# Performance work log

Measured on AMD Instinct MI355X. Metric: run time of the kernel, lower is better.

## Reference

```python
import jax, jax.numpy as jnp
import numpy as np

N_CTX = 4096
D_MODEL = 2048
D_HEAD = 128


def setup_inputs() -> dict:
    key = jax.random.key(0)
    k1, k2, k3, k4 = jax.random.split(key, 4)
    x = jax.random.normal(k1, (N_CTX, D_MODEL), dtype=jnp.float32)
    # torch nn.Linear weights are [out, in]; kept in that layout.
    Wk = jax.random.normal(k2, (D_HEAD, D_MODEL), dtype=jnp.float32) * (1.0 / np.sqrt(D_MODEL))
    Wq = jax.random.normal(k3, (D_HEAD, D_MODEL), dtype=jnp.float32) * (1.0 / np.sqrt(D_MODEL))
    W2 = jax.random.normal(k4, (D_MODEL, D_MODEL), dtype=jnp.float32) * (1.0 / np.sqrt(D_MODEL))
    return {"x": x, "Wk": Wk, "Wq": Wq, "W2": W2}


def reference(x, Wk, Wq, W2):
    # Faithful to the torch module: no 1/sqrt(d_head) scaling, V = x itself.
    n = x.shape[0]
    q = x @ Wq.T                     # [n, d_head]
    k = x @ Wk.T                     # [n, d_head]
    scores = q @ k.T                 # [n, n]
    # causal mask: strictly-upper-triangular entries -> -inf
    causal = jnp.tril(jnp.ones((n, n), dtype=bool))
    scores = jnp.where(causal, scores, -jnp.inf)
    attn = jax.nn.softmax(scores, axis=1)  # [n, n]
    out = attn @ x                   # [n, d_model] (V is the raw input)
    return out @ W2.T                # [n, d_model]
```

## Files before the change

kernel.cpp:

```cpp
#include <hip/hip_runtime.h>

#define NCTX 4096
#define DMODEL 2048
#define DHEAD 128

typedef _Float16 f16;
typedef f16 f16x8 __attribute__((ext_vector_type(8)));
typedef float f32x4 __attribute__((ext_vector_type(4)));
typedef unsigned short u16;
typedef u16 u16x8 __attribute__((ext_vector_type(8)));

__device__ __forceinline__ u16 f2h(float f) {
  union { f16 h; u16 u; } v; v.h = (f16)f; return v.u;
}
__device__ __forceinline__ float h2f(u16 u) {
  union { u16 u; f16 h; } v; v.u = u; return (float)v.h;
}

__device__ __forceinline__ void gl_lds16(const void* g, void* l) {
  __builtin_amdgcn_global_load_lds((const __attribute__((address_space(1))) void*)g,
                                   (__attribute__((address_space(3))) void*)l, 16, 0, 0);
}

__device__ __forceinline__ void splitH4(float4 v, ushort4& h, ushort4& l) {
  h.x = f2h(v.x); l.x = f2h(v.x - h2f(h.x));
  h.y = f2h(v.y); l.y = f2h(v.y - h2f(h.y));
  h.z = f2h(v.z); l.z = f2h(v.z - h2f(h.z));
  h.w = f2h(v.w); l.w = f2h(v.w - h2f(h.w));
}

__global__ __launch_bounds__(256) void prep_all(const float* __restrict__ x,
                                                const float* __restrict__ Wq,
                                                const float* __restrict__ Wk,
                                                const float* __restrict__ W2,
                                                u16* __restrict__ xh, u16* __restrict__ xl,
                                                u16* __restrict__ Wf, u16* __restrict__ W2f,
                                                u16* __restrict__ XT) {
  __shared__ float tile[64][65];
  int b = blockIdx.x;
  int t = threadIdx.x;
  if (b < 2048) {
    int mb = (b >> 5) * 64, db = (b & 31) * 64;
    int tx = t & 15, ty = t >> 4;
#pragma unroll
    for (int rr = 0; rr < 4; ++rr) {
      int row = rr * 16 + ty;
      float4 v = *(const float4*)(x + (size_t)(mb + row) * DMODEL + db + tx * 4);
      ushort4 h, l; splitH4(v, h, l);
      size_t gi = ((size_t)(mb + row) * DMODEL + db) / 4 + tx;
      ((ushort4*)xh)[gi] = h; ((ushort4*)xl)[gi] = l;
      tile[row][tx * 4 + 0] = v.x; tile[row][tx * 4 + 1] = v.y;
      tile[row][tx * 4 + 2] = v.z; tile[row][tx * 4 + 3] = v.w;
    }
    __syncthreads();
#pragma unroll
    for (int rr = 0; rr < 4; ++rr) {
      int r = (t >> 4) * 4 + rr;
      int c0 = (t & 15) * 4;
      ushort4 o;
      o.x = f2h(tile[c0 + 0][r]); o.y = f2h(tile[c0 + 1][r]);
      o.z = f2h(tile[c0 + 2][r]); o.w = f2h(tile[c0 + 3][r]);
      *(ushort4*)(XT + (size_t)(db + r) * NCTX + mb + c0) = o;
    }
  } else if (b < 2560) {
    int wk = (b >= 2304);
    int i = (b - (wk ? 2304 : 2048)) * 256 + t;
    const float* W = wk ? Wk : Wq;
    size_t off = wk ? ((size_t)DHEAD * DMODEL / 4) : 0;
    float4 v = ((const float4*)W)[i];
    ushort4 o;
    o.x = f2h(v.x); o.y = f2h(v.y); o.z = f2h(v.z); o.w = f2h(v.w);
    ((ushort4*)Wf)[off + i] = o;
  } else {
    int i = (b - 2560) * 256 + t;
    float4 v = ((const float4*)W2)[i];
    ushort4 o;
    o.x = f2h(v.x); o.y = f2h(v.y); o.z = f2h(v.z); o.w = f2h(v.w);
    ((ushort4*)W2f)[i] = o;
  }
}

__global__ __launch_bounds__(256) void reduce8h(const u16* __restrict__ P,
                                                u16* __restrict__ out, int n8) {
  int i = blockIdx.x * 256 + threadIdx.x;
  if (i >= n8) return;
  float s[8] = {};
#pragma unroll
  for (int z = 0; z < 8; ++z) {
    u16x8 v = ((const u16x8*)P)[(size_t)z * n8 + i];
#pragma unroll
    for (int k = 0; k < 8; ++k) s[k] += h2f(v[k]);
  }
  u16x8 o;
#pragma unroll
  for (int k = 0; k < 8; ++k) o[k] = f2h(s[k]);
  ((u16x8*)out)[i] = o;
}

__global__ __launch_bounds__(256) void reduce_c2(const u16* __restrict__ P,
                                                 u16* __restrict__ out, size_t cs) {
  int row = 2048 + blockIdx.x;
  int t = threadIdx.x;
  size_t base = (size_t)row * DMODEL + t * 8;
  u16x8 a = *(const u16x8*)(P + base);
  u16x8 b = *(const u16x8*)(P + cs + base);
  u16x8 o;
#pragma unroll
  for (int k = 0; k < 8; ++k) o[k] = f2h(h2f(a[k]) + h2f(b[k]));
  *(u16x8*)(out + base) = o;
}

__global__ __launch_bounds__(256) void softmax_wave(const float* __restrict__ S,
                                                    u16* __restrict__ P) {
  int t = threadIdx.x;
  int lane = t & 63, w = t >> 6;
  int row = blockIdx.x * 4 + w;
  const float* srow = S + (size_t)row * NCTX;
  int len = row + 1;
  int jmax = ((row >> 7) + 1) << 7;
  float4 v[16];
  float mx = -3.0e38f;
#pragma unroll
  for (int k = 0; k < 16; ++k) {
    int j = k * 256 + lane * 4;
    if (j < jmax) {
      float4 x = *(const float4*)(srow + j);
      x.x = (j + 0 < len) ? x.x : -3.0e38f;
      x.y = (j + 1 < len) ? x.y : -3.0e38f;
      x.z = (j + 2 < len) ? x.z : -3.0e38f;
      x.w = (j + 3 < len) ? x.w : -3.0e38f;
      v[k] = x;
      mx = fmaxf(mx, fmaxf(fmaxf(x.x, x.y), fmaxf(x.z, x.w)));
    }
  }
#pragma unroll
  for (int o = 32; o > 0; o >>= 1) mx = fmaxf(mx, __shfl_xor(mx, o, 64));
  float sum = 0.f;
#pragma unroll
  for (int k = 0; k < 16; ++k) {
    int j = k * 256 + lane * 4;
    if (j < jmax) {
      float4 x = v[k];
      x.x = (j + 0 < len) ? __expf(x.x - mx) : 0.f;
      x.y = (j + 1 < len) ? __expf(x.y - mx) : 0.f;
      x.z = (j + 2 < len) ? __expf(x.z - mx) : 0.f;
      x.w = (j + 3 < len) ? __expf(x.w - mx) : 0.f;
      v[k] = x;
      sum += x.x + x.y + x.z + x.w;
    }
  }
#pragma unroll
  for (int o = 32; o > 0; o >>= 1) sum += __shfl_xor(sum, o, 64);
  float inv = 1.0f / sum;
  u16* prow = P + (size_t)row * NCTX;
#pragma unroll
  for (int k = 0; k < 16; ++k) {
    int j = k * 256 + lane * 4;
    if (j < jmax) {
      float4 x = v[k];
      ushort4 o4;
      o4.x = f2h(x.x * inv); o4.y = f2h(x.y * inv);
      o4.z = f2h(x.z * inv); o4.w = f2h(x.w * inv);
      *(ushort4*)(prow + j) = o4;
    }
  }
}

__global__ __launch_bounds__(256, 4) void gemm_f16_p(const u16* __restrict__ A,
                                                     const u16* __restrict__ B,
                                                     float* __restrict__ C,
                                                     int lda, int ldb, int ldc,
                                                     int K, int KC, size_t chunkStride,
                                                     int causal, int tri) {
  int bm = gridDim.x - 1 - blockIdx.x, bn = blockIdx.y, kc = blockIdx.z;
  if (tri && bn > bm) return;
  int kEnd = K;
  if (causal) { int ke = (bm + 1) * 128; if (ke < kEnd) kEnd = ke; }
  int kStart = kc * KC;
  if (kStart >= kEnd) return;
  int kStop = kStart + KC < kEnd ? kStart + KC : kEnd;
  __shared__ __align__(16) u16 As[128 * 64];
  __shared__ __align__(16) u16 Bs[128 * 64];
  int t = threadIdx.x;
  int lane = t & 63, w = t >> 6;
  int m0 = bm * 128, n0 = bn * 128;
  int wm = (w >> 1) * 64, wn = (w & 1) * 64;
  int mfrag = lane & 15, quad = lane >> 4;
  int srow = t >> 3, schunk = t & 7;
  int rsw = mfrag & 7;
  f32x4 acc[4][4] = {};
  for (int kt = kStart; kt < kStop; kt += 64) {
#pragma unroll
    for (int p = 0; p < 4; ++p) {
      int row = p * 32 + srow;
      int gsc = schunk ^ (row & 7);
      gl_lds16(A + (size_t)(m0 + row) * lda + kt + gsc * 8, As + (size_t)(p * 256 + t) * 8);
      gl_lds16(B + (size_t)(n0 + row) * ldb + kt + gsc * 8, Bs + (size_t)(p * 256 + t) * 8);
    }
    __syncthreads();
#pragma unroll
    for (int ks = 0; ks < 2; ++ks) {
      int c0 = ((ks * 4 + quad) ^ rsw) * 8;
      f16x8 af[4], bfr[4];
#pragma unroll
      for (int i = 0; i < 4; ++i)
        af[i] = *(const f16x8*)(As + (wm + i * 16 + mfrag) * 64 + c0);
#pragma unroll
      for (int j = 0; j < 4; ++j)
        bfr[j] = *(const f16x8*)(Bs + (wn + j * 16 + mfrag) * 64 + c0);
#pragma unroll
      for (int i = 0; i < 4; ++i)
#pragma unroll
        for (int j = 0; j < 4; ++j)
          acc[i][j] = __builtin_amdgcn_mfma_f32_16x16x32_f16(af[i], bfr[j], acc[i][j], 0, 0, 0);
    }
    __syncthreads();
  }
  float* Cc = C + (size_t)kc * chunkStride;
#pragma unroll
  for (int i = 0; i < 4; ++i)
#pragma unroll
    for (int j = 0; j < 4; ++j)
#pragma unroll
      for (int rr = 0; rr < 4; ++rr) {
        int row = m0 + wm + i * 16 + quad * 4 + rr;
        int col = n0 + wn + j * 16 + mfrag;
        Cc[(size_t)row * ldc + col] = acc[i][j][rr];
      }
}

__global__ __launch_bounds__(256, 4) void gemm_attnx(const u16* __restrict__ A,
                                                     const u16* __restrict__ B,
                                                     u16* __restrict__ C,
                                                     u16* __restrict__ Cf,
                                                     size_t chunkStride) {
  int b = blockIdx.x;
  int s = b >> 8, c = b & 255;
  int r = (s == 0) ? c : (s == 1) ? (511 - c) : (512 + c);
  int bm, bn, kc;
  if (r < 272) {
    bm = 15 + (r >> 4); bn = r & 15; kc = 0;
  } else if (r < 288) {
    bm = 31; bn = r - 272; kc = 1;
  } else {
    int g = (r - 288) >> 5, j = (r - 288) & 31;
    int k = 15 - g;
    if (j < 16) { bm = k - 1; bn = j; kc = 0; }
    else        { bm = 15 + k; bn = j - 16; kc = 1; }
  }
  int kEnd = (bm + 1) * 128;
  if (kEnd > NCTX) kEnd = NCTX;
  int kStart = kc * 2048;
  int kStop = kStart + 2048 < kEnd ? kStart + 2048 : kEnd;
  __shared__ __align__(16) u16 As[128 * 64];
  __shared__ __align__(16) u16 Bs[128 * 64];
  int t = threadIdx.x;
  int lane = t & 63, w = t >> 6;
  int m0 = bm * 128, n0 = bn * 128;
  int wm = (w >> 1) * 64, wn = (w & 1) * 64;
  int mfrag = lane & 15, quad = lane >> 4;
  int srow = t >> 3, schunk = t & 7;
  int rsw = mfrag & 7;
  f32x4 acc[4][4] = {};
  for (int kt = kStart; kt < kStop; kt += 64) {
#pragma unroll
    for (int p = 0; p < 4; ++p) {
      int row = p * 32 + srow;
      int gsc = schunk ^ (row & 7);
      gl_lds16(A + (size_t)(m0 + row) * NCTX + kt + gsc * 8, As + (size_t)(p * 256 + t) * 8);
      gl_lds16(B + (size_t)(n0 + row) * NCTX + kt + gsc * 8, Bs + (size_t)(p * 256 + t) * 8);
    }
    __syncthreads();
#pragma unroll
    for (int ks = 0; ks < 2; ++ks) {
      int c0 = ((ks * 4 + quad) ^ rsw) * 8;
      f16x8 af[4], bfr[4];
#pragma unroll
      for (int i = 0; i < 4; ++i)
        af[i] = *(const f16x8*)(As + (wm + i * 16 + mfrag) * 64 + c0);
#pragma unroll
      for (int j = 0; j < 4; ++j)
        bfr[j] = *(const f16x8*)(Bs + (wn + j * 16 + mfrag) * 64 + c0);
#pragma unroll
      for (int i = 0; i < 4; ++i)
#pragma unroll
        for (int j = 0; j < 4; ++j)
          acc[i][j] = __builtin_amdgcn_mfma_f32_16x16x32_f16(af[i], bfr[j], acc[i][j], 0, 0, 0);
    }
    __syncthreads();
  }
  u16* Cc = (kc == 0 && kEnd <= 2048) ? Cf : (C + (size_t)kc * chunkStride);
#pragma unroll
  for (int i = 0; i < 4; ++i)
#pragma unroll
    for (int j = 0; j < 4; ++j)
#pragma unroll
      for (int rr = 0; rr < 4; ++rr) {
        int row = m0 + wm + i * 16 + quad * 4 + rr;
        int col = n0 + wn + j * 16 + mfrag;
        Cc[(size_t)row * DMODEL + col] = f2h(acc[i][j][rr]);
      }
}

__global__ __launch_bounds__(256, 3) void gemm_f16x2_p(const u16* __restrict__ Ah,
                                                       const u16* __restrict__ Al,
                                                       const u16* __restrict__ B,
                                                       u16* __restrict__ C,
                                                       int lda, int ldb, int ldc,
                                                       int K, int KC, size_t chunkStride) {
  int bm = blockIdx.x, bn = blockIdx.y, kc = blockIdx.z;
  int kStart = kc * KC;
  int kStop = kStart + KC < K ? kStart + KC : K;
  __shared__ __align__(16) u16 Ash[128 * 64];
  __shared__ __align__(16) u16 Asl[128 * 64];
  __shared__ __align__(16) u16 Bs[128 * 64];
  int t = threadIdx.x;
  int lane = t & 63, w = t >> 6;
  int m0 = bm * 128, n0 = bn * 128;
  int wm = (w >> 1) * 64, wn = (w & 1) * 64;
  int mfrag = lane & 15, quad = lane >> 4;
  int srow = t >> 3, schunk = t & 7;
  int rsw = mfrag & 7;
  f32x4 acc[4][4] = {};
  for (int kt = kStart; kt < kStop; kt += 64) {
#pragma unroll
    for (int p = 0; p < 4; ++p) {
      int row = p * 32 + srow;
      int gsc = schunk ^ (row & 7);
      size_t aoff = (size_t)(m0 + row) * lda + kt + gsc * 8;
      size_t loff = (size_t)(p * 256 + t) * 8;
      gl_lds16(Ah + aoff, Ash + loff);
      gl_lds16(Al + aoff, Asl + loff);
      gl_lds16(B + (size_t)(n0 + row) * ldb + kt + gsc * 8, Bs + loff);
    }
    __syncthreads();
#pragma unroll
    for (int ks = 0; ks < 2; ++ks) {
      int c0 = ((ks * 4 + quad) ^ rsw) * 8;
      f16x8 a0[4], bfr[4];
#pragma unroll
      for (int j = 0; j < 4; ++j)
        bfr[j] = *(const f16x8*)(Bs + (wn + j * 16 + mfrag) * 64 + c0);
#pragma unroll
      for (int i = 0; i < 4; ++i)
        a0[i] = *(const f16x8*)(Ash + (wm + i * 16 + mfrag) * 64 + c0);
#pragma unroll
      for (int i = 0; i < 4; ++i)
#pragma unroll
        for (int j = 0; j < 4; ++j)
          acc[i][j] = __builtin_amdgcn_mfma_f32_16x16x32_f16(a0[i], bfr[j], acc[i][j], 0, 0, 0);
#pragma unroll
      for (int i = 0; i < 4; ++i)
        a0[i] = *(const f16x8*)(Asl + (wm + i * 16 + mfrag) * 64 + c0);
#pragma unroll
      for (int i = 0; i < 4; ++i)
#pragma unroll
        for (int j = 0; j < 4; ++j)
          acc[i][j] = __builtin_amdgcn_mfma_f32_16x16x32_f16(a0[i], bfr[j], acc[i][j], 0, 0, 0);
    }
    __syncthreads();
  }
  u16* Cc = C + (size_t)kc * chunkStride;
#pragma unroll
  for (int i = 0; i < 4; ++i)
#pragma unroll
    for (int j = 0; j < 4; ++j)
#pragma unroll
      for (int rr = 0; rr < 4; ++rr) {
        int row = m0 + wm + i * 16 + quad * 4 + rr;
        int col = n0 + wn + j * 16 + mfrag;
        Cc[(size_t)row * ldc + col] = f2h(acc[i][j][rr]);
      }
}

extern "C" void kernel_launch(void* const* d_in, const int* in_sizes, int n_in,
                              void* d_out, int out_size, void* d_ws, size_t ws_size,
                              hipStream_t stream) {
  const float* x  = (const float*)d_in[0];
  const float* Wk = (const float*)d_in[1];
  const float* Wq = (const float*)d_in[2];
  const float* W2 = (const float*)d_in[3];

  char* ws = (char*)d_ws;
  const size_t MB = 1024 * 1024;
  u16*   QKf  = (u16*)  (ws + 0);
  u16*   Wf   = (u16*)  (ws + 2 * MB);
  u16*   xT   = (u16*)  (ws + 3 * MB);
  u16*   W2f  = (u16*)  (ws + 19 * MB);
  u16*   outb = (u16*)  (ws + 27 * MB);
  u16*   attn = (u16*)  (ws + 43 * MB);
  u16*   xh   = (u16*)  (ws + 75 * MB);
  u16*   xl   = (u16*)  (ws + 91 * MB);
  u16*   QKp  = (u16*)  (ws + 107 * MB);
  float* S    = (float*)(ws + 75 * MB);
  u16*   Ph   = (u16*)  (ws + 75 * MB);

  const int QKN8 = NCTX * 256 / 8;
  const size_t CS = (size_t)NCTX * DMODEL;

  prep_all<<<6656, 256, 0, stream>>>(x, Wq, Wk, W2, xh, xl, Wf, W2f, xT);

  gemm_f16x2_p<<<dim3(NCTX / 128, 2, 8), 256, 0, stream>>>(
      xh, xl, Wf, QKp, DMODEL, DMODEL, 256, DMODEL, 256, (size_t)NCTX * 256);
  reduce8h<<<(QKN8 + 255) / 256, 256, 0, stream>>>(QKp, QKf, QKN8);

  gemm_f16_p<<<dim3(NCTX / 128, NCTX / 128, 1), 256, 0, stream>>>(
      QKf, QKf + DHEAD, S, 256, 256, NCTX, DHEAD, DHEAD, 0, 0, 1);
  softmax_wave<<<1024, 256, 0, stream>>>(S, attn);

  gemm_attnx<<<768, 256, 0, stream>>>(attn, xT, Ph, outb, CS);
  reduce_c2<<<2048, 256, 0, stream>>>(Ph, outb, CS);

  gemm_f16_p<<<dim3(NCTX / 128, DMODEL / 128, 1), 256, 0, stream>>>(
      outb, W2f, (float*)d_out, DMODEL, DMODEL, DMODEL, DMODEL, DMODEL, 0, 0, 0);
}
```

Baseline: 225.9 us.

## Fuse split-K reduction into W2 GEMM and compact triangular scores grid

Removes the reduce_c2 kernel by having the final W2 GEMM load and add the two partial attn@x halves directly while staging A tiles for the lower rows. The scores GEMM becomes a specialised kernel launched over only the 528 lower-triangular tiles, using an index-to-(bm,bn) mapping instead of early-returning blocks, with a fixed K loop. This saves one launch and a round trip of the partial sums through memory. In exchange, the hi-half blocks of the W2 GEMM use synchronous register loads instead of async global-to-LDS loads, which may slow them.

```diff
diff --git a/kernel.cpp b/kernel.cpp
--- a/kernel.cpp
+++ b/kernel.cpp
@@ -97,19 +97,6 @@
   ((u16x8*)out)[i] = o;
 }
 
-__global__ __launch_bounds__(256) void reduce_c2(const u16* __restrict__ P,
-                                                 u16* __restrict__ out, size_t cs) {
-  int row = 2048 + blockIdx.x;
-  int t = threadIdx.x;
-  size_t base = (size_t)row * DMODEL + t * 8;
-  u16x8 a = *(const u16x8*)(P + base);
-  u16x8 b = *(const u16x8*)(P + cs + base);
-  u16x8 o;
-#pragma unroll
-  for (int k = 0; k < 8; ++k) o[k] = f2h(h2f(a[k]) + h2f(b[k]));
-  *(u16x8*)(out + base) = o;
-}
-
 __global__ __launch_bounds__(256) void softmax_wave(const float* __restrict__ S,
                                                     u16* __restrict__ P) {
   int t = threadIdx.x;
@@ -166,19 +153,14 @@
   }
 }
 
-__global__ __launch_bounds__(256, 4) void gemm_f16_p(const u16* __restrict__ A,
-                                                     const u16* __restrict__ B,
-                                                     float* __restrict__ C,
-                                                     int lda, int ldb, int ldc,
-                                                     int K, int KC, size_t chunkStride,
-                                                     int causal, int tri) {
-  int bm = gridDim.x - 1 - blockIdx.x, bn = blockIdx.y, kc = blockIdx.z;
-  if (tri && bn > bm) return;
-  int kEnd = K;
-  if (causal) { int ke = (bm + 1) * 128; if (ke < kEnd) kEnd = ke; }
-  int kStart = kc * KC;
-  if (kStart >= kEnd) return;
-  int kStop = kStart + KC < kEnd ? kStart + KC : kEnd;
+__global__ __launch_bounds__(256, 4) void gemm_scores(const u16* __restrict__ A,
+                                                      const u16* __restrict__ B,
+                                                      float* __restrict__ C) {
+  int q = blockIdx.x;
+  int bm = (int)((sqrtf(8.0f * (float)q + 1.0f) - 1.0f) * 0.5f);
+  while ((bm + 1) * (bm + 2) / 2 <= q) ++bm;
+  while (bm * (bm + 1) / 2 > q) --bm;
+  int bn = q - bm * (bm + 1) / 2;
   __shared__ __align__(16) u16 As[128 * 64];
   __shared__ __align__(16) u16 Bs[128 * 64];
   int t = threadIdx.x;
@@ -189,13 +171,14 @@
   int srow = t >> 3, schunk = t & 7;
   int rsw = mfrag & 7;
   f32x4 acc[4][4] = {};
-  for (int kt = kStart; kt < kStop; kt += 64) {
+#pragma unroll
+  for (int kt = 0; kt < 128; kt += 64) {
 #pragma unroll
     for (int p = 0; p < 4; ++p) {
       int row = p * 32 + srow;
       int gsc = schunk ^ (row & 7);
-      gl_lds16(A + (size_t)(m0 + row) * lda + kt + gsc * 8, As + (size_t)(p * 256 + t) * 8);
-      gl_lds16(B + (size_t)(n0 + row) * ldb + kt + gsc * 8, Bs + (size_t)(p * 256 + t) * 8);
+      gl_lds16(A + (size_t)(m0 + row) * 256 + kt + gsc * 8, As + (size_t)(p * 256 + t) * 8);
+      gl_lds16(B + (size_t)(n0 + row) * 256 + kt + gsc * 8, Bs + (size_t)(p * 256 + t) * 8);
     }
     __syncthreads();
 #pragma unroll
@@ -216,7 +199,6 @@
     }
     __syncthreads();
   }
-  float* Cc = C + (size_t)kc * chunkStride;
 #pragma unroll
   for (int i = 0; i < 4; ++i)
 #pragma unroll
@@ -225,7 +207,7 @@
       for (int rr = 0; rr < 4; ++rr) {
         int row = m0 + wm + i * 16 + quad * 4 + rr;
         int col = n0 + wn + j * 16 + mfrag;
-        Cc[(size_t)row * ldc + col] = acc[i][j][rr];
+        C[(size_t)row * NCTX + col] = acc[i][j][rr];
       }
 }
 
@@ -302,6 +284,81 @@
       }
 }
 
+__global__ __launch_bounds__(256, 4) void gemm_w2(const u16* __restrict__ Ad,
+                                                  const u16* __restrict__ Ph0,
+                                                  const u16* __restrict__ Ph1,
+                                                  const u16* __restrict__ B,
+                                                  float* __restrict__ C) {
+  int bm = blockIdx.x, bn = blockIdx.y;
+  __shared__ __align__(16) u16 As[128 * 64];
+  __shared__ __align__(16) u16 Bs[128 * 64];
+  int t = threadIdx.x;
+  int lane = t & 63, w = t >> 6;
+  int m0 = bm * 128, n0 = bn * 128;
+  int wm = (w >> 1) * 64, wn = (w & 1) * 64;
+  int mfrag = lane & 15, quad = lane >> 4;
+  int srow = t >> 3, schunk = t & 7;
+  int rsw = mfrag & 7;
+  int hi = (m0 >= 2048);
+  f32x4 acc[4][4] = {};
+  for (int kt = 0; kt < DMODEL; kt += 64) {
+    if (hi) {
+      f16x8 va[4], vb[4];
+#pragma unroll
+      for (int p = 0; p < 4; ++p) {
+        int row = p * 32 + srow;
+        int gsc = schunk ^ (row & 7);
+        size_t off = (size_t)(m0 + row) * DMODEL + kt + gsc * 8;
+        va[p] = *(const f16x8*)((const f16*)Ph0 + off);
+        vb[p] = *(const f16x8*)((const f16*)Ph1 + off);
+        gl_lds16(B + (size_t)(n0 + row) * DMODEL + kt + gsc * 8,
+                 Bs + (size_t)(p * 256 + t) * 8);
+      }
+#pragma unroll
+      for (int p = 0; p < 4; ++p)
+        *(f16x8*)(As + (size_t)(p * 256 + t) * 8) = va[p] + vb[p];
+    } else {
+#pragma unroll
+      for (int p = 0; p < 4; ++p) {
+        int row = p * 32 + srow;
+        int gsc = schunk ^ (row & 7);
+        gl_lds16(Ad + (size_t)(m0 + row) * DMODEL + kt + gsc * 8,
+                 As + (size_t)(p * 256 + t) * 8);
+        gl_lds16(B + (size_t)(n0 + row) * DMODEL + kt + gsc * 8,
+                 Bs + (size_t)(p * 256 + t) * 8);
+      }
+    }
+    __syncthreads();
+#pragma unroll
+    for (int ks = 0; ks < 2; ++ks) {
+      int c0 = ((ks * 4 + quad) ^ rsw) * 8;
+      f16x8 af[4], bfr[4];
+#pragma unroll
+      for (int i = 0; i < 4; ++i)
+        af[i] = *(const f16x8*)(As + (wm + i * 16 + mfrag) * 64 + c0);
+#pragma unroll
+      for (int j = 0; j < 4; ++j)
+        bfr[j] = *(const f16x8*)(Bs + (wn + j * 16 + mfrag) * 64 + c0);
+#pragma unroll
+      for (int i = 0; i < 4; ++i)
+#pragma unroll
+        for (int j = 0; j < 4; ++j)
+          acc[i][j] = __builtin_amdgcn_mfma_f32_16x16x32_f16(af[i], bfr[j], acc[i][j], 0, 0, 0);
+    }
+    __syncthreads();
+  }
+#pragma unroll
+  for (int i = 0; i < 4; ++i)
+#pragma unroll
+    for (int j = 0; j < 4; ++j)
+#pragma unroll
+      for (int rr = 0; rr < 4; ++rr) {
+        int row = m0 + wm + i * 16 + quad * 4 + rr;
+        int col = n0 + wn + j * 16 + mfrag;
+        C[(size_t)row * DMODEL + col] = acc[i][j][rr];
+      }
+}
+
 __global__ __launch_bounds__(256, 3) void gemm_f16x2_p(const u16* __restrict__ Ah,
                                                        const u16* __restrict__ Al,
                                                        const u16* __restrict__ B,
@@ -404,13 +461,11 @@
       xh, xl, Wf, QKp, DMODEL, DMODEL, 256, DMODEL, 256, (size_t)NCTX * 256);
   reduce8h<<<(QKN8 + 255) / 256, 256, 0, stream>>>(QKp, QKf, QKN8);
 
-  gemm_f16_p<<<dim3(NCTX / 128, NCTX / 128, 1), 256, 0, stream>>>(
-      QKf, QKf + DHEAD, S, 256, 256, NCTX, DHEAD, DHEAD, 0, 0, 1);
+  gemm_scores<<<528, 256, 0, stream>>>(QKf, QKf + DHEAD, S);
   softmax_wave<<<1024, 256, 0, stream>>>(S, attn);
 
   gemm_attnx<<<768, 256, 0, stream>>>(attn, xT, Ph, outb, CS);
-  reduce_c2<<<2048, 256, 0, stream>>>(Ph, outb, CS);
-
-  gemm_f16_p<<<dim3(NCTX / 128, DMODEL / 128, 1), 256, 0, stream>>>(
-      outb, W2f, (float*)d_out, DMODEL, DMODEL, DMODEL, DMODEL, DMODEL, 0, 0, 0);
-}
+
+  gemm_w2<<<dim3(NCTX / 128, DMODEL / 128), 256, 0, stream>>>(
+      outb, Ph, Ph + CS, W2f, (float*)d_out);
+}
```

New measurement: 301.3 us. +33.4%, slower.
